# Performance work log

Hardware: AMD Instinct MI355X
Metric: run time of the kernel (lower is better)

## Reference

```python
import jax, jax.numpy as jnp
import numpy as np


def setup_inputs() -> dict:
    key = jax.random.key(0)
    k1, k2 = jax.random.split(key)
    B, L, D = 16, 1024, 256
    sentence1 = jax.random.normal(k1, (B, L, D), dtype=jnp.float32)
    sentence2 = jax.random.normal(k2, (B, L, D), dtype=jnp.float32)
    return {"batch_size": B, "sentence1": sentence1, "sentence2": sentence2}


def reference(batch_size, sentence1, sentence2):
    # A[k,i,j] = 1 / (1 + ||s1[k,i] - s2[k,j]||_2)
    # materializing the [B, L1, L2, D] difference tensor.
    x2 = jnp.sum(sentence1 * sentence1, axis=-1)          # [B, L1]
    y2 = jnp.sum(sentence2 * sentence2, axis=-1)          # [B, L2]
    xy = jnp.einsum("bid,bjd->bij", sentence1, sentence2)  # [B, L1, L2]
    sq = x2[:, :, None] + y2[:, None, :] - 2.0 * xy
    sq = jnp.maximum(sq, 0.0)  # guard tiny negatives from cancellation
    dist = jnp.sqrt(sq)
    return 1.0 / (1.0 + dist)
```

## Files before the change

kernel.cpp:

```cpp
#include <hip/hip_runtime.h>
#include <hip/hip_bf16.h>

typedef __attribute__((ext_vector_type(4))) float f32x4;
typedef __attribute__((ext_vector_type(8))) __bf16 bf16x8;
typedef __attribute__((ext_vector_type(4))) __bf16 bf16x4;

#define B_DIM 16
#define L_DIM 1024
#define D_DIM 256

#define GLOAD_LDS16(g, lptr)                                          \
    __builtin_amdgcn_global_load_lds(                                 \
        (const __attribute__((address_space(1))) void*)(g),           \
        (__attribute__((address_space(3))) void*)(lptr), 16, 0, 0)

#define SBAR() __builtin_amdgcn_sched_barrier(0)

__global__ __launch_bounds__(256) void prep_kernel(const float* __restrict__ s1,
                                                   const float* __restrict__ s2,
                                                   float* __restrict__ nrm,
                                                   __hip_bfloat16* __restrict__ s1b,
                                                   __hip_bfloat16* __restrict__ s2b) {
    const int w = threadIdx.x >> 6, l = threadIdx.x & 63;
    const int base = (blockIdx.x << 4) + (w << 2);
#pragma unroll
    for (int i = 0; i < 4; ++i) {
        const int row = base + i;
        const int second = row >> 14;
        const int r = row & 16383;
        const float* src = (second ? s2 : s1) + (size_t)r * D_DIM;
        __hip_bfloat16* dst = (second ? s2b : s1b) + (size_t)r * D_DIM;
        float4 v = reinterpret_cast<const float4*>(src)[l];
        float s = v.x * v.x + v.y * v.y + v.z * v.z + v.w * v.w;
        bf16x4 bv;
        bv[0] = (__bf16)v.x; bv[1] = (__bf16)v.y; bv[2] = (__bf16)v.z; bv[3] = (__bf16)v.w;
        *reinterpret_cast<bf16x4*>(dst + l * 4) = bv;
#pragma unroll
        for (int o = 32; o > 0; o >>= 1) s += __shfl_xor(s, o, 64);
        if (l == 0) nrm[row] = s;
    }
}

__global__ __launch_bounds__(256, 2) void dist_gemm2_kernel(const __hip_bfloat16* __restrict__ s1b,
                                                            const __hip_bfloat16* __restrict__ s2b,
                                                            const float* __restrict__ nrm,
                                                            float* __restrict__ out) {
    __shared__ __bf16 Alds[4][128 * 32];
    __shared__ __bf16 Blds[4][128 * 32];

    const int t = threadIdx.x;
    const int p = blockIdx.x;
    const int d = ((p & 7) << 6) + (p >> 3);
    const int batch = d >> 5;
    const int rem = d & 31;
    const int row0 = (rem >> 2) << 7;
    const int col0a = (rem & 3) << 8;
    const int col0b = col0a + 128;

    const __hip_bfloat16* Ag = s1b + ((size_t)batch * L_DIM + row0) * D_DIM;
    const __hip_bfloat16* Bg0 = s2b + ((size_t)batch * L_DIM + col0a) * D_DIM;
    const __hip_bfloat16* Bg1 = s2b + ((size_t)batch * L_DIM + col0b) * D_DIM;

    const int l = t & 63, w = t >> 6;
    const int wr = w >> 1, wc = w & 1;
    const int lr = l & 15;
    const int lq = l >> 4;

    const int srow_in_seg = l >> 2;
    const int sslot = (l & 3) ^ ((l >> 3) & 3);

    auto stageK = [&](const __hip_bfloat16* Bg, int kt) {
        const int k0 = kt << 5;
        const int b = kt & 3;
#pragma unroll
        for (int i = 0; i < 2; ++i) {
            const int s = (w << 1) | i;
            const int rl = (s << 4) + srow_in_seg;
            GLOAD_LDS16(Ag + rl * D_DIM + k0 + sslot * 8, &Alds[b][s << 9]);
            GLOAD_LDS16(Bg + rl * D_DIM + k0 + sslot * 8, &Blds[b][s << 9]);
        }
    };

    bf16x8 aF[2][4], bF[2][4];
    auto readFrags = [&](int kt, bf16x8* a, bf16x8* bfr) {
        const int b = kt & 3;
#pragma unroll
        for (int m = 0; m < 4; ++m) {
            const int row = (wr << 6) + (m << 4) + lr;
            const int sl = lq ^ ((row >> 1) & 3);
            a[m] = *reinterpret_cast<const bf16x8*>(&Alds[b][(row << 5) + (sl << 3)]);
        }
#pragma unroll
        for (int n = 0; n < 4; ++n) {
            const int row = (wc << 6) + (n << 4) + lr;
            const int sl = lq ^ ((row >> 1) & 3);
            bfr[n] = *reinterpret_cast<const bf16x8*>(&Blds[b][(row << 5) + (sl << 3)]);
        }
    };

    const float* x2 = nrm + batch * L_DIM;
    const float* y2 = nrm + B_DIM * L_DIM + batch * L_DIM;
    const int rbase = row0 + (wr << 6) + (lq << 2);
    const int cloc = (wc << 6) + lr;

    float* outb = out + (size_t)batch * L_DIM * L_DIM;
    auto epilogue = [&](const f32x4 (&acc)[4][4], const f32x4 (&xv)[4],
                        const float (&yv)[4], int col0_) {
        const int cb = col0_ + cloc;
#pragma unroll
        for (int n = 0; n < 4; ++n) {
            const int col = cb + (n << 4);
            const float y2v = yv[n];
#pragma unroll
            for (int m = 0; m < 4; ++m) {
#pragma unroll
                for (int r = 0; r < 4; ++r) {
                    const int row = rbase + (m << 4) + r;
                    float sq = xv[m][r] + y2v - 2.0f * acc[m][n][r];
                    sq = fmaxf(sq, 0.0f);
                    float den = 1.0f + __builtin_amdgcn_sqrtf(sq);
                    outb[(size_t)row * L_DIM + col] = __builtin_amdgcn_rcpf(den);
                }
            }
        }
    };

    f32x4 acc0[4][4] = {};
    stageK(Bg0, 0); stageK(Bg0, 1); stageK(Bg0, 2);
    SBAR();
    f32x4 xv[4]; float yv0[4];
#pragma unroll
    for (int m = 0; m < 4; ++m) xv[m] = *reinterpret_cast<const f32x4*>(&x2[rbase + (m << 4)]);
#pragma unroll
    for (int n = 0; n < 4; ++n) yv0[n] = y2[col0a + cloc + (n << 4)];
    SBAR();
    asm volatile("s_waitcnt vmcnt(12)" ::: "memory");
    __builtin_amdgcn_s_barrier();
    readFrags(0, aF[0], bF[0]);

#pragma unroll
    for (int kt = 0; kt < 8; ++kt) {
        if (kt == 1)      asm volatile("s_waitcnt vmcnt(12)" ::: "memory");
        else if (kt >= 2 && kt <= 5) asm volatile("s_waitcnt vmcnt(4)" ::: "memory");
        else if (kt >= 6) asm volatile("s_waitcnt vmcnt(0)" ::: "memory");
        if (kt >= 1) __builtin_amdgcn_s_barrier();
        if (kt < 7) readFrags(kt + 1, aF[(kt + 1) & 1], bF[(kt + 1) & 1]);
        if (kt < 7) asm volatile("s_waitcnt lgkmcnt(8)" ::: "memory");
        else        asm volatile("s_waitcnt lgkmcnt(0)" ::: "memory");
        if (kt <= 4) stageK(Bg0, kt + 3);
        __builtin_amdgcn_s_setprio(1);
#pragma unroll
        for (int m = 0; m < 4; ++m)
#pragma unroll
            for (int n = 0; n < 4; ++n)
                acc0[m][n] = __builtin_amdgcn_mfma_f32_16x16x32_bf16(
                    aF[kt & 1][m], bF[kt & 1][n], acc0[m][n], 0, 0, 0);
        __builtin_amdgcn_s_setprio(0);
    }

    stageK(Bg1, 0); stageK(Bg1, 1); stageK(Bg1, 2);
    SBAR();
    float yv1[4];
#pragma unroll
    for (int n = 0; n < 4; ++n) yv1[n] = y2[col0b + cloc + (n << 4)];
    SBAR();
    epilogue(acc0, xv, yv0, col0a);
    SBAR();
    asm volatile("s_waitcnt vmcnt(24)" ::: "memory");
    __builtin_amdgcn_s_barrier();

    f32x4 acc1[4][4] = {};
    readFrags(0, aF[0], bF[0]);

#pragma unroll
    for (int kt = 0; kt < 8; ++kt) {
        if (kt == 1)      asm volatile("s_waitcnt vmcnt(24)" ::: "memory");
        else if (kt >= 2 && kt <= 5) asm volatile("s_waitcnt vmcnt(4)" ::: "memory");
        else if (kt >= 6) asm volatile("s_waitcnt vmcnt(0)" ::: "memory");
        if (kt >= 1) __builtin_amdgcn_s_barrier();
        if (kt < 7) readFrags(kt + 1, aF[(kt + 1) & 1], bF[(kt + 1) & 1]);
        if (kt < 7) asm volatile("s_waitcnt lgkmcnt(8)" ::: "memory");
        else        asm volatile("s_waitcnt lgkmcnt(0)" ::: "memory");
        if (kt <= 4) stageK(Bg1, kt + 3);
        __builtin_amdgcn_s_setprio(1);
#pragma unroll
        for (int m = 0; m < 4; ++m)
#pragma unroll
            for (int n = 0; n < 4; ++n)
                acc1[m][n] = __builtin_amdgcn_mfma_f32_16x16x32_bf16(
                    aF[kt & 1][m], bF[kt & 1][n], acc1[m][n], 0, 0, 0);
        __builtin_amdgcn_s_setprio(0);
    }

    epilogue(acc1, xv, yv1, col0b);
}

__global__ __launch_bounds__(256) void norms_kernel(const float* __restrict__ s1,
                                                    const float* __restrict__ s2,
                                                    float* __restrict__ nrm) {
    int w = threadIdx.x >> 6, l = threadIdx.x & 63;
    int row = (blockIdx.x << 2) + w;
    const float* src = (row < B_DIM * L_DIM)
                           ? (s1 + (size_t)row * D_DIM)
                           : (s2 + (size_t)(row - B_DIM * L_DIM) * D_DIM);
    float4 v = reinterpret_cast<const float4*>(src)[l];
    float s = v.x * v.x + v.y * v.y + v.z * v.z + v.w * v.w;
#pragma unroll
    for (int o = 32; o > 0; o >>= 1) s += __shfl_xor(s, o, 64);
    if (l == 0) nrm[row] = s;
}

__global__ __launch_bounds__(256) void dist_gemm_kernel(const float* __restrict__ s1,
                                                        const float* __restrict__ s2,
                                                        const float* __restrict__ nrm,
                                                        float* __restrict__ out) {
    __shared__ __bf16 Alds[2][128 * 32];
    __shared__ __bf16 Blds[2][128 * 32];

    const int t = threadIdx.x;
    const int p = blockIdx.x;
    const int d = ((p & 7) << 7) + (p >> 3);
    const int batch = d >> 6;
    const int tile = d & 63;
    const int row0 = (tile >> 3) << 7;
    const int col0 = (tile & 7) << 7;

    const float* Ag = s1 + ((size_t)batch * L_DIM + row0) * D_DIM;
    const float* Bg = s2 + ((size_t)batch * L_DIM + col0) * D_DIM;

    const int sr = t >> 2;
    const int sc = (t & 3) << 3;

    const int l = t & 63, w = t >> 6;
    const int wr = w >> 1, wc = w & 1;
    const int lr = l & 15;
    const int lk = (l >> 4) << 3;

    f32x4 acc[4][4] = {};

    auto stage = [&](int buf, int k0) {
#pragma unroll
        for (int pass = 0; pass < 2; ++pass) {
            const int r = sr + (pass << 6);
            const float4* sa = reinterpret_cast<const float4*>(Ag + (size_t)r * D_DIM + k0 + sc);
            float4 a0 = sa[0], a1 = sa[1];
            const float4* sb = reinterpret_cast<const float4*>(Bg + (size_t)r * D_DIM + k0 + sc);
            float4 b0 = sb[0], b1 = sb[1];
            bf16x8 av, bv;
            av[0] = (__bf16)a0.x; av[1] = (__bf16)a0.y; av[2] = (__bf16)a0.z; av[3] = (__bf16)a0.w;
            av[4] = (__bf16)a1.x; av[5] = (__bf16)a1.y; av[6] = (__bf16)a1.z; av[7] = (__bf16)a1.w;
            bv[0] = (__bf16)b0.x; bv[1] = (__bf16)b0.y; bv[2] = (__bf16)b0.z; bv[3] = (__bf16)b0.w;
            bv[4] = (__bf16)b1.x; bv[5] = (__bf16)b1.y; bv[6] = (__bf16)b1.z; bv[7] = (__bf16)b1.w;
            *reinterpret_cast<bf16x8*>(&Alds[buf][(r << 5) + sc]) = av;
            *reinterpret_cast<bf16x8*>(&Blds[buf][(r << 5) + sc]) = bv;
        }
    };

    stage(0, 0);
    __syncthreads();
    int cur = 0;
    for (int kt = 0; kt < 8; ++kt) {
        if (kt < 7) stage(cur ^ 1, (kt + 1) << 5);
        bf16x8 aF[4], bF[4];
#pragma unroll
        for (int m = 0; m < 4; ++m)
            aF[m] = *reinterpret_cast<const bf16x8*>(
                &Alds[cur][(((wr << 6) + (m << 4) + lr) << 5) + lk]);
#pragma unroll
        for (int n = 0; n < 4; ++n)
            bF[n] = *reinterpret_cast<const bf16x8*>(
                &Blds[cur][(((wc << 6) + (n << 4) + lr) << 5) + lk]);
#pragma unroll
        for (int m = 0; m < 4; ++m)
#pragma unroll
            for (int n = 0; n < 4; ++n)
                acc[m][n] = __builtin_amdgcn_mfma_f32_16x16x32_bf16(aF[m], bF[n], acc[m][n], 0, 0, 0);
        __syncthreads();
        cur ^= 1;
    }

    const float* x2 = nrm + batch * L_DIM;
    const float* y2 = nrm + B_DIM * L_DIM + batch * L_DIM;
    float* outb = out + (size_t)batch * L_DIM * L_DIM;
    const int rbase = row0 + (wr << 6) + ((l >> 4) << 2);
    const int cbase = col0 + (wc << 6) + lr;
#pragma unroll
    for (int n = 0; n < 4; ++n) {
        const int col = cbase + (n << 4);
        const float y2v = y2[col];
#pragma unroll
        for (int m = 0; m < 4; ++m) {
            const int rowf = rbase + (m << 4);
#pragma unroll
            for (int r = 0; r < 4; ++r) {
                const int row = rowf + r;
                float sq = x2[row] + y2v - 2.0f * acc[m][n][r];
                sq = fmaxf(sq, 0.0f);
                outb[(size_t)row * L_DIM + col] = 1.0f / (1.0f + sqrtf(sq));
            }
        }
    }
}

extern "C" void kernel_launch(void* const* d_in, const int* in_sizes, int n_in,
                              void* d_out, int out_size, void* d_ws, size_t ws_size,
                              hipStream_t stream) {
    (void)in_sizes; (void)n_in; (void)out_size;
    const float* s1 = (const float*)d_in[1];
    const float* s2 = (const float*)d_in[2];
    float* out = (float*)d_out;

    const size_t NRM_BYTES = 2u * B_DIM * L_DIM * sizeof(float);
    const size_t BF_BYTES = (size_t)B_DIM * L_DIM * D_DIM * sizeof(__hip_bfloat16);
    const size_t NEED = NRM_BYTES + 2 * BF_BYTES;

    float* nrm = (float*)d_ws;
    if (ws_size >= NEED) {
        __hip_bfloat16* s1b = (__hip_bfloat16*)((char*)d_ws + NRM_BYTES);
        __hip_bfloat16* s2b = (__hip_bfloat16*)((char*)d_ws + NRM_BYTES + BF_BYTES);
        prep_kernel<<<2048, 256, 0, stream>>>(s1, s2, nrm, s1b, s2b);
        dist_gemm2_kernel<<<512, 256, 0, stream>>>(s1b, s2b, nrm, out);
    } else {
        norms_kernel<<<8192, 256, 0, stream>>>(s1, s2, nrm);
        dist_gemm_kernel<<<1024, 256, 0, stream>>>(s1, s2, nrm, out);
    }
}
```

Baseline: 32.17 us.

## Interleave first tile's epilogue stores into second tile's MFMA loop

The epilogue for the first output tile is split into eight slices, and each slice runs inside one iteration of the second tile's K loop, so its global stores overlap with MFMA work instead of stalling between the two GEMMs. All norm loads are hoisted ahead of the first staging. The vmcnt wait thresholds are retuned to count the in-flight stores. This keeps acc0 live during the second GEMM, which raises register pressure, and the hand-set vmcnt counts must match the real number of outstanding memory ops to stay correct.

```diff
diff --git a/kernel.cpp b/kernel.cpp
--- a/kernel.cpp
+++ b/kernel.cpp
@@ -102,48 +102,47 @@
     const float* y2 = nrm + B_DIM * L_DIM + batch * L_DIM;
     const int rbase = row0 + (wr << 6) + (lq << 2);
     const int cloc = (wc << 6) + lr;
-
     float* outb = out + (size_t)batch * L_DIM * L_DIM;
-    auto epilogue = [&](const f32x4 (&acc)[4][4], const f32x4 (&xv)[4],
-                        const float (&yv)[4], int col0_) {
-        const int cb = col0_ + cloc;
-#pragma unroll
-        for (int n = 0; n < 4; ++n) {
-            const int col = cb + (n << 4);
+
+    auto epiSlice = [&](const f32x4 (&acc)[4][4], const f32x4 (&xv)[4],
+                        const float* yv, int col0_, int s) {
+#pragma unroll
+        for (int j = 2 * s; j < 2 * s + 2; ++j) {
+            const int n = j >> 2, m = j & 3;
+            const int col = col0_ + cloc + (n << 4);
             const float y2v = yv[n];
 #pragma unroll
-            for (int m = 0; m < 4; ++m) {
-#pragma unroll
-                for (int r = 0; r < 4; ++r) {
-                    const int row = rbase + (m << 4) + r;
-                    float sq = xv[m][r] + y2v - 2.0f * acc[m][n][r];
-                    sq = fmaxf(sq, 0.0f);
-                    float den = 1.0f + __builtin_amdgcn_sqrtf(sq);
-                    outb[(size_t)row * L_DIM + col] = __builtin_amdgcn_rcpf(den);
-                }
+            for (int r = 0; r < 4; ++r) {
+                const int row = rbase + (m << 4) + r;
+                float sq = fmaxf(xv[m][r] + y2v - 2.0f * acc[m][n][r], 0.0f);
+                outb[(size_t)row * L_DIM + col] =
+                    __builtin_amdgcn_rcpf(1.0f + __builtin_amdgcn_sqrtf(sq));
             }
         }
     };
 
+    f32x4 xv[4]; float yv0[4], yv1[4];
+#pragma unroll
+    for (int m = 0; m < 4; ++m) xv[m] = *reinterpret_cast<const f32x4*>(&x2[rbase + (m << 4)]);
+#pragma unroll
+    for (int n = 0; n < 4; ++n) yv0[n] = y2[col0a + cloc + (n << 4)];
+#pragma unroll
+    for (int n = 0; n < 4; ++n) yv1[n] = y2[col0b + cloc + (n << 4)];
+    SBAR();
     f32x4 acc0[4][4] = {};
     stageK(Bg0, 0); stageK(Bg0, 1); stageK(Bg0, 2);
     SBAR();
-    f32x4 xv[4]; float yv0[4];
-#pragma unroll
-    for (int m = 0; m < 4; ++m) xv[m] = *reinterpret_cast<const f32x4*>(&x2[rbase + (m << 4)]);
-#pragma unroll
-    for (int n = 0; n < 4; ++n) yv0[n] = y2[col0a + cloc + (n << 4)];
-    SBAR();
-    asm volatile("s_waitcnt vmcnt(12)" ::: "memory");
+    asm volatile("s_waitcnt vmcnt(4)" ::: "memory");
     __builtin_amdgcn_s_barrier();
     readFrags(0, aF[0], bF[0]);
 
 #pragma unroll
     for (int kt = 0; kt < 8; ++kt) {
-        if (kt == 1)      asm volatile("s_waitcnt vmcnt(12)" ::: "memory");
-        else if (kt >= 2 && kt <= 5) asm volatile("s_waitcnt vmcnt(4)" ::: "memory");
-        else if (kt >= 6) asm volatile("s_waitcnt vmcnt(0)" ::: "memory");
-        if (kt >= 1) __builtin_amdgcn_s_barrier();
+        if (kt >= 1) {
+            if (kt <= 5) asm volatile("s_waitcnt vmcnt(4)" ::: "memory");
+            else         asm volatile("s_waitcnt vmcnt(0)" ::: "memory");
+            __builtin_amdgcn_s_barrier();
+        }
         if (kt < 7) readFrags(kt + 1, aF[(kt + 1) & 1], bF[(kt + 1) & 1]);
         if (kt < 7) asm volatile("s_waitcnt lgkmcnt(8)" ::: "memory");
         else        asm volatile("s_waitcnt lgkmcnt(0)" ::: "memory");
@@ -160,23 +159,16 @@
 
     stageK(Bg1, 0); stageK(Bg1, 1); stageK(Bg1, 2);
     SBAR();
-    float yv1[4];
-#pragma unroll
-    for (int n = 0; n < 4; ++n) yv1[n] = y2[col0b + cloc + (n << 4)];
-    SBAR();
-    epilogue(acc0, xv, yv0, col0a);
-    SBAR();
-    asm volatile("s_waitcnt vmcnt(24)" ::: "memory");
+    asm volatile("s_waitcnt vmcnt(4)" ::: "memory");
     __builtin_amdgcn_s_barrier();
-
     f32x4 acc1[4][4] = {};
     readFrags(0, aF[0], bF[0]);
 
 #pragma unroll
     for (int kt = 0; kt < 8; ++kt) {
-        if (kt == 1)      asm volatile("s_waitcnt vmcnt(24)" ::: "memory");
-        else if (kt >= 2 && kt <= 5) asm volatile("s_waitcnt vmcnt(4)" ::: "memory");
-        else if (kt >= 6) asm volatile("s_waitcnt vmcnt(0)" ::: "memory");
+        if (kt == 1)      asm volatile("s_waitcnt vmcnt(12)" ::: "memory");
+        else if (kt >= 2 && kt <= 5) asm volatile("s_waitcnt vmcnt(20)" ::: "memory");
+        else if (kt == 6) asm volatile("s_waitcnt vmcnt(16)" ::: "memory");
         if (kt >= 1) __builtin_amdgcn_s_barrier();
         if (kt < 7) readFrags(kt + 1, aF[(kt + 1) & 1], bF[(kt + 1) & 1]);
         if (kt < 7) asm volatile("s_waitcnt lgkmcnt(8)" ::: "memory");
@@ -190,9 +182,11 @@
                 acc1[m][n] = __builtin_amdgcn_mfma_f32_16x16x32_bf16(
                     aF[kt & 1][m], bF[kt & 1][n], acc1[m][n], 0, 0, 0);
         __builtin_amdgcn_s_setprio(0);
-    }
-
-    epilogue(acc1, xv, yv1, col0b);
+        epiSlice(acc0, xv, yv0, col0a, kt);
+    }
+
+#pragma unroll
+    for (int s = 0; s < 8; ++s) epiSlice(acc1, xv, yv1, col0b, s);
 }
 
 __global__ __launch_bounds__(256) void norms_kernel(const float* __restrict__ s1,
```

Result: slower. 34.06 us (+5.9%).

## Load A fragments directly from global into registers, dropping A LDS staging

Applied to the files above, without the earlier changes.

The GEMM kernel no longer stages the s1 tile through shared memory. Each wave now loads its A fragments straight from global memory into a triple-buffered register array, two k-steps ahead, while B keeps the LDS path. The intent is to cut the LDS footprint in half and remove the A LDS reads, which could allow more blocks per CU and ease LDS traffic. In exchange, A is read redundantly by both column waves, register pressure goes up, and the vmcnt wait accounting has to be retuned.

```diff
diff --git a/kernel.cpp b/kernel.cpp
--- a/kernel.cpp
+++ b/kernel.cpp
@@ -45,7 +45,6 @@
                                                             const __hip_bfloat16* __restrict__ s2b,
                                                             const float* __restrict__ nrm,
                                                             float* __restrict__ out) {
-    __shared__ __bf16 Alds[4][128 * 32];
     __shared__ __bf16 Blds[4][128 * 32];
 
     const int t = threadIdx.x;
@@ -57,7 +56,6 @@
     const int col0a = (rem & 3) << 8;
     const int col0b = col0a + 128;
 
-    const __hip_bfloat16* Ag = s1b + ((size_t)batch * L_DIM + row0) * D_DIM;
     const __hip_bfloat16* Bg0 = s2b + ((size_t)batch * L_DIM + col0a) * D_DIM;
     const __hip_bfloat16* Bg1 = s2b + ((size_t)batch * L_DIM + col0b) * D_DIM;
 
@@ -66,30 +64,35 @@
     const int lr = l & 15;
     const int lq = l >> 4;
 
+    const __hip_bfloat16* Abase =
+        s1b + ((size_t)batch * L_DIM + row0 + (wr << 6) + lr) * D_DIM + (lq << 3);
+
     const int srow_in_seg = l >> 2;
     const int sslot = (l & 3) ^ ((l >> 3) & 3);
 
-    auto stageK = [&](const __hip_bfloat16* Bg, int kt) {
+    auto stageB = [&](const __hip_bfloat16* Bg, int kt) {
         const int k0 = kt << 5;
         const int b = kt & 3;
 #pragma unroll
         for (int i = 0; i < 2; ++i) {
             const int s = (w << 1) | i;
             const int rl = (s << 4) + srow_in_seg;
-            GLOAD_LDS16(Ag + rl * D_DIM + k0 + sslot * 8, &Alds[b][s << 9]);
             GLOAD_LDS16(Bg + rl * D_DIM + k0 + sslot * 8, &Blds[b][s << 9]);
         }
     };
 
-    bf16x8 aF[2][4], bF[2][4];
-    auto readFrags = [&](int kt, bf16x8* a, bf16x8* bfr) {
+    bf16x8 aA[3][4];
+    auto loadA = [&](int kt) {
+        const int ko = kt << 5;
+        bf16x8* dst = aA[kt % 3];
+#pragma unroll
+        for (int m = 0; m < 4; ++m)
+            dst[m] = *reinterpret_cast<const bf16x8*>(Abase + (size_t)(m << 4) * D_DIM + ko);
+    };
+
+    bf16x8 bF[2][4];
+    auto readFragsB = [&](int kt, bf16x8* bfr) {
         const int b = kt & 3;
-#pragma unroll
-        for (int m = 0; m < 4; ++m) {
-            const int row = (wr << 6) + (m << 4) + lr;
-            const int sl = lq ^ ((row >> 1) & 3);
-            a[m] = *reinterpret_cast<const bf16x8*>(&Alds[b][(row << 5) + (sl << 3)]);
-        }
 #pragma unroll
         for (int n = 0; n < 4; ++n) {
             const int row = (wc << 6) + (n << 4) + lr;
@@ -102,8 +105,8 @@
     const float* y2 = nrm + B_DIM * L_DIM + batch * L_DIM;
     const int rbase = row0 + (wr << 6) + (lq << 2);
     const int cloc = (wc << 6) + lr;
-
     float* outb = out + (size_t)batch * L_DIM * L_DIM;
+
     auto epilogue = [&](const f32x4 (&acc)[4][4], const f32x4 (&xv)[4],
                         const float (&yv)[4], int col0_) {
         const int cb = col0_ + cloc;
@@ -116,79 +119,85 @@
 #pragma unroll
                 for (int r = 0; r < 4; ++r) {
                     const int row = rbase + (m << 4) + r;
-                    float sq = xv[m][r] + y2v - 2.0f * acc[m][n][r];
-                    sq = fmaxf(sq, 0.0f);
-                    float den = 1.0f + __builtin_amdgcn_sqrtf(sq);
-                    outb[(size_t)row * L_DIM + col] = __builtin_amdgcn_rcpf(den);
+                    float sq = fmaxf(xv[m][r] + y2v - 2.0f * acc[m][n][r], 0.0f);
+                    outb[(size_t)row * L_DIM + col] =
+                        __builtin_amdgcn_rcpf(1.0f + __builtin_amdgcn_sqrtf(sq));
                 }
             }
         }
     };
 
+    f32x4 xv[4]; float yv0[4], yv1[4];
+#pragma unroll
+    for (int m = 0; m < 4; ++m) xv[m] = *reinterpret_cast<const f32x4*>(&x2[rbase + (m << 4)]);
+#pragma unroll
+    for (int n = 0; n < 4; ++n) yv0[n] = y2[col0a + cloc + (n << 4)];
+#pragma unroll
+    for (int n = 0; n < 4; ++n) yv1[n] = y2[col0b + cloc + (n << 4)];
+    SBAR();
+    loadA(0); loadA(1);
+    SBAR();
     f32x4 acc0[4][4] = {};
-    stageK(Bg0, 0); stageK(Bg0, 1); stageK(Bg0, 2);
-    SBAR();
-    f32x4 xv[4]; float yv0[4];
-#pragma unroll
-    for (int m = 0; m < 4; ++m) xv[m] = *reinterpret_cast<const f32x4*>(&x2[rbase + (m << 4)]);
-#pragma unroll
-    for (int n = 0; n < 4; ++n) yv0[n] = y2[col0a + cloc + (n << 4)];
-    SBAR();
-    asm volatile("s_waitcnt vmcnt(12)" ::: "memory");
+    stageB(Bg0, 0); stageB(Bg0, 1); stageB(Bg0, 2);
+    SBAR();
+    asm volatile("s_waitcnt vmcnt(2)" ::: "memory");
     __builtin_amdgcn_s_barrier();
-    readFrags(0, aF[0], bF[0]);
+    readFragsB(0, bF[0]);
 
 #pragma unroll
     for (int kt = 0; kt < 8; ++kt) {
-        if (kt == 1)      asm volatile("s_waitcnt vmcnt(12)" ::: "memory");
-        else if (kt >= 2 && kt <= 5) asm volatile("s_waitcnt vmcnt(4)" ::: "memory");
-        else if (kt >= 6) asm volatile("s_waitcnt vmcnt(0)" ::: "memory");
-        if (kt >= 1) __builtin_amdgcn_s_barrier();
-        if (kt < 7) readFrags(kt + 1, aF[(kt + 1) & 1], bF[(kt + 1) & 1]);
-        if (kt < 7) asm volatile("s_waitcnt lgkmcnt(8)" ::: "memory");
+        if (kt >= 1) {
+            if (kt <= 5)      asm volatile("s_waitcnt vmcnt(6)" ::: "memory");
+            else if (kt == 6) asm volatile("s_waitcnt vmcnt(4)" ::: "memory");
+            else              asm volatile("s_waitcnt vmcnt(0)" ::: "memory");
+            __builtin_amdgcn_s_barrier();
+        }
+        if (kt < 7) readFragsB(kt + 1, bF[(kt + 1) & 1]);
+        if (kt < 7) asm volatile("s_waitcnt lgkmcnt(4)" ::: "memory");
         else        asm volatile("s_waitcnt lgkmcnt(0)" ::: "memory");
-        if (kt <= 4) stageK(Bg0, kt + 3);
+        if (kt <= 5) loadA(kt + 2);
+        if (kt <= 4) stageB(Bg0, kt + 3);
         __builtin_amdgcn_s_setprio(1);
 #pragma unroll
         for (int m = 0; m < 4; ++m)
 #pragma unroll
             for (int n = 0; n < 4; ++n)
                 acc0[m][n] = __builtin_amdgcn_mfma_f32_16x16x32_bf16(
-                    aF[kt & 1][m], bF[kt & 1][n], acc0[m][n], 0, 0, 0);
+                    aA[kt % 3][m], bF[kt & 1][n], acc0[m][n], 0, 0, 0);
         __builtin_amdgcn_s_setprio(0);
     }
 
-    stageK(Bg1, 0); stageK(Bg1, 1); stageK(Bg1, 2);
-    SBAR();
-    float yv1[4];
-#pragma unroll
-    for (int n = 0; n < 4; ++n) yv1[n] = y2[col0b + cloc + (n << 4)];
+    stageB(Bg1, 0); stageB(Bg1, 1); stageB(Bg1, 2);
+    SBAR();
+    loadA(0); loadA(1);
     SBAR();
     epilogue(acc0, xv, yv0, col0a);
     SBAR();
-    asm volatile("s_waitcnt vmcnt(24)" ::: "memory");
+    asm volatile("s_waitcnt vmcnt(63)" ::: "memory");
     __builtin_amdgcn_s_barrier();
-
     f32x4 acc1[4][4] = {};
-    readFrags(0, aF[0], bF[0]);
+    readFragsB(0, bF[0]);
 
 #pragma unroll
     for (int kt = 0; kt < 8; ++kt) {
-        if (kt == 1)      asm volatile("s_waitcnt vmcnt(24)" ::: "memory");
-        else if (kt >= 2 && kt <= 5) asm volatile("s_waitcnt vmcnt(4)" ::: "memory");
-        else if (kt >= 6) asm volatile("s_waitcnt vmcnt(0)" ::: "memory");
-        if (kt >= 1) __builtin_amdgcn_s_barrier();
-        if (kt < 7) readFrags(kt + 1, aF[(kt + 1) & 1], bF[(kt + 1) & 1]);
-        if (kt < 7) asm volatile("s_waitcnt lgkmcnt(8)" ::: "memory");
+        if (kt >= 1) {
+            if (kt >= 2 && kt <= 5) asm volatile("s_waitcnt vmcnt(6)" ::: "memory");
+            else if (kt == 6)       asm volatile("s_waitcnt vmcnt(4)" ::: "memory");
+            else if (kt == 7)       asm volatile("s_waitcnt vmcnt(0)" ::: "memory");
+            __builtin_amdgcn_s_barrier();
+        }
+        if (kt < 7) readFragsB(kt + 1, bF[(kt + 1) & 1]);
+        if (kt < 7) asm volatile("s_waitcnt lgkmcnt(4)" ::: "memory");
         else        asm volatile("s_waitcnt lgkmcnt(0)" ::: "memory");
-        if (kt <= 4) stageK(Bg1, kt + 3);
+        if (kt <= 5) loadA(kt + 2);
+        if (kt <= 4) stageB(Bg1, kt + 3);
         __builtin_amdgcn_s_setprio(1);
 #pragma unroll
         for (int m = 0; m < 4; ++m)
 #pragma unroll
             for (int n = 0; n < 4; ++n)
                 acc1[m][n] = __builtin_amdgcn_mfma_f32_16x16x32_bf16(
-                    aF[kt & 1][m], bF[kt & 1][n], acc1[m][n], 0, 0, 0);
+                    aA[kt % 3][m], bF[kt & 1][n], acc1[m][n], 0, 0, 0);
         __builtin_amdgcn_s_setprio(0);
     }
 
@@ -215,7 +224,7 @@
                                                         const float* __restrict__ nrm,
                                                         float* __restrict__ out) {
     __shared__ __bf16 Alds[2][128 * 32];
-    __shared__ __bf16 Blds[2][128 * 32];
+    __shared__ __bf16 Blds2[2][128 * 32];
 
     const int t = threadIdx.x;
     const int p = blockIdx.x;
@@ -252,7 +261,7 @@
             bv[0] = (__bf16)b0.x; bv[1] = (__bf16)b0.y; bv[2] = (__bf16)b0.z; bv[3] = (__bf16)b0.w;
             bv[4] = (__bf16)b1.x; bv[5] = (__bf16)b1.y; bv[6] = (__bf16)b1.z; bv[7] = (__bf16)b1.w;
             *reinterpret_cast<bf16x8*>(&Alds[buf][(r << 5) + sc]) = av;
-            *reinterpret_cast<bf16x8*>(&Blds[buf][(r << 5) + sc]) = bv;
+            *reinterpret_cast<bf16x8*>(&Blds2[buf][(r << 5) + sc]) = bv;
         }
     };
 
@@ -269,7 +278,7 @@
 #pragma unroll
         for (int n = 0; n < 4; ++n)
             bF[n] = *reinterpret_cast<const bf16x8*>(
-                &Blds[cur][(((wc << 6) + (n << 4) + lr) << 5) + lk]);
+                &Blds2[cur][(((wc << 6) + (n << 4) + lr) << 5) + lk]);
 #pragma unroll
         for (int m = 0; m < 4; ++m)
 #pragma unroll
```

Measured after the change: 38.11 us. 1.18x slower.
